# Kernel optimization log

Measured on AMD Instinct MI355X. Metric: run time of the kernel, lower is better.

The kernel has to match this reference:

```python
import jax, jax.numpy as jnp
import numpy as np


def setup_inputs() -> dict:
    key = jax.random.key(0)
    k1, k2 = jax.random.split(key)
    x = jax.random.normal(k1, (32, 64, 64, 64), dtype=jnp.float32)      # (B, D, H, W)
    weight = jax.random.uniform(k2, (64, 512), dtype=jnp.float32)       # (D, K), like torch.rand
    return {"x": x, "weight": weight}


def reference(x, weight):
    # Euclidean nearest-embedding (hyperbolic=False, bounded_measure=False).
    # argmin of ||x - e||_2 over codebook equals argmin of squared distance;
    # drop the ||x||^2 term (constant per location) for efficiency.
    # x: (B, D, H, W), weight: (D, K)
    scores = -2.0 * jnp.einsum('bdhw,dk->bhwk', x, weight) + jnp.sum(weight * weight, axis=0)  # (B,H,W,K)
    argmin = jnp.argmin(scores, axis=-1)                 # (B, H, W) int
    quantized = weight.T[argmin]                         # (B, H, W, D) codebook gather
    result = jnp.transpose(quantized, (0, 3, 1, 2))      # (B, D, H, W)
    return result, argmin
```

## Files before the change

kernel.cpp:

```cpp
#include <hip/hip_runtime.h>


typedef float  f32x4  __attribute__((ext_vector_type(4)));
typedef short  bf16x8 __attribute__((ext_vector_type(8)));

#define KK   512
#define DD   64
#define HWSZ 4096
#define NLOC (32*HWSZ)
#define LPB  512
#define TAU  1e-3f

static __device__ __forceinline__ short f2bf_rne(float f) {
    unsigned u = __float_as_uint(f);
    unsigned r = (u + 0x7FFFu + ((u >> 16) & 1u)) >> 16;
    return (short)r;
}

__global__ __launch_bounds__(1024, 4)
void ne_mfma(const float* __restrict__ x, const float* __restrict__ w,
             float* __restrict__ out_res, float* __restrict__ out_idx) {
    __shared__ __align__(16) short wt_hi[KK*DD];
    __shared__ __align__(16) short wt_lo[KK*DD];
    __shared__ __align__(16) float w2s[KK];
    __shared__ int k1s[LPB];

    const int tid  = threadIdx.x;
    const int lane = tid & 63;
    const int wv   = tid >> 6;
    const int col  = lane & 15;
    const int lgr  = lane >> 4;

    const int bloc0 = blockIdx.x * LPB;
    const int b     = bloc0 >> 12;
    const long xbase = (long)b * (DD*HWSZ);
    const int hw0   = bloc0 & 4095;

    char* wh_b = (char*)wt_hi;
    char* wl_b = (char*)wt_lo;

    {
        const int n = tid & 511;
        const int h = tid >> 9;
        #pragma unroll
        for (int gg = 0; gg < 4; ++gg) {
            const int g = h*4 + gg;
            bf16x8 hv, lv;
            #pragma unroll
            for (int j = 0; j < 8; ++j) {
                float v = w[(g*8 + j)*KK + n];
                unsigned bits = __float_as_uint(v);
                unsigned hb = bits & 0xFFFF0000u;
                hv[j] = (short)(hb >> 16);
                lv[j] = f2bf_rne(v - __uint_as_float(hb));
            }
            const int slot = g ^ (n & 7);
            *(bf16x8*)(wh_b + n*128 + slot*16) = hv;
            *(bf16x8*)(wl_b + n*128 + slot*16) = lv;
        }
        if (h == 0) {
            float w2 = 0.f;
            #pragma unroll
            for (int d = 0; d < DD; ++d) {
                float v = w[d*KK + n];
                w2 = fmaf(v, v, w2);
            }
            w2s[n] = w2;
        }
    }

    const int wloc0 = bloc0 + wv * 32;
    bf16x8 Xh0[2], Xl0[2], Xh1[2], Xl1[2];
    #pragma unroll
    for (int s = 0; s < 2; ++s) {
        const int hw = (wloc0 + s*16 + col) & 4095;
        #pragma unroll
        for (int c = 0; c < 2; ++c) {
            #pragma unroll
            for (int j = 0; j < 8; ++j) {
                const int d = c*32 + lgr*8 + j;
                float v = x[xbase + (long)d*HWSZ + hw];
                unsigned bits = __float_as_uint(v);
                unsigned hb = bits & 0xFFFF0000u;
                short hj = (short)(hb >> 16);
                short lj = f2bf_rne(v - __uint_as_float(hb));
                if (s == 0) { Xh0[c][j] = hj; Xl0[c][j] = lj; }
                else        { Xh1[c][j] = hj; Xl1[c][j] = lj; }
            }
        }
    }

    __syncthreads();

    float m1[2][4], m2[2][4]; int i1[2][4], i2[2][4];
    #pragma unroll
    for (int s = 0; s < 2; ++s)
        #pragma unroll
        for (int r = 0; r < 4; ++r) { m1[s][r] = 3.4e38f; m2[s][r] = 3.4e38f; i1[s][r] = 0; i2[s][r] = 0; }

    #pragma unroll 2
    for (int t = 0; t < 32; ++t) {
        const int n = t*16 + col;
        f32x4 acc0 = {0.f,0.f,0.f,0.f}, acc1 = {0.f,0.f,0.f,0.f};
        #pragma unroll
        for (int c = 0; c < 2; ++c) {
            const int off = (n*128 + (c*4 + lgr)*16) ^ ((n & 7) << 4);
            bf16x8 Wh = *(const bf16x8*)(wh_b + off);
            bf16x8 Wl = *(const bf16x8*)(wl_b + off);
            acc0 = __builtin_amdgcn_mfma_f32_16x16x32_bf16(Wl, Xh0[c], acc0, 0,0,0);
            acc0 = __builtin_amdgcn_mfma_f32_16x16x32_bf16(Wh, Xl0[c], acc0, 0,0,0);
            acc0 = __builtin_amdgcn_mfma_f32_16x16x32_bf16(Wh, Xh0[c], acc0, 0,0,0);
            acc1 = __builtin_amdgcn_mfma_f32_16x16x32_bf16(Wl, Xh1[c], acc1, 0,0,0);
            acc1 = __builtin_amdgcn_mfma_f32_16x16x32_bf16(Wh, Xl1[c], acc1, 0,0,0);
            acc1 = __builtin_amdgcn_mfma_f32_16x16x32_bf16(Wh, Xh1[c], acc1, 0,0,0);
        }
        const f32x4 w2v = *(const f32x4*)((const char*)w2s + t*64 + lgr*16);
        const int kb = t*16 + lgr*4;
        #pragma unroll
        for (int r = 0; r < 4; ++r) {
            {
                float sc = fmaf(-2.f, acc0[r], w2v[r]);
                bool c1 = sc < m1[0][r], c2 = sc < m2[0][r];
                m2[0][r] = c1 ? m1[0][r] : (c2 ? sc : m2[0][r]);
                i2[0][r] = c1 ? i1[0][r] : (c2 ? (kb+r) : i2[0][r]);
                m1[0][r] = c1 ? sc : m1[0][r];
                i1[0][r] = c1 ? (kb+r) : i1[0][r];
            }
            {
                float sc = fmaf(-2.f, acc1[r], w2v[r]);
                bool c1 = sc < m1[1][r], c2 = sc < m2[1][r];
                m2[1][r] = c1 ? m1[1][r] : (c2 ? sc : m2[1][r]);
                i2[1][r] = c1 ? i1[1][r] : (c2 ? (kb+r) : i2[1][r]);
                m1[1][r] = c1 ? sc : m1[1][r];
                i1[1][r] = c1 ? (kb+r) : i1[1][r];
            }
        }
    }

    #pragma unroll
    for (int s = 0; s < 2; ++s) {
        float a1 = m1[s][0], a2 = m2[s][0]; int j1 = i1[s][0], j2 = i2[s][0];
        #pragma unroll
        for (int r = 1; r < 4; ++r) {
            float b1v = m1[s][r], b2v = m2[s][r]; int jb1 = i1[s][r], jb2 = i2[s][r];
            bool bw = (b1v < a1) || (b1v == a1 && jb1 < j1);
            float w1 = bw ? b1v : a1;  int wj1 = bw ? jb1 : j1;
            float lo = bw ? a1  : b1v; int loj = bw ? j1  : jb1;
            float ws = bw ? b2v : a2;  int wsj = bw ? jb2 : j2;
            bool sw = (lo < ws) || (lo == ws && loj < wsj);
            a1 = w1; j1 = wj1;
            a2 = sw ? lo : ws; j2 = sw ? loj : wsj;
        }
        #pragma unroll
        for (int msk = 16; msk <= 32; msk <<= 1) {
            float b1v = __shfl_xor(a1, msk, 64);
            int   jb1 = __shfl_xor(j1, msk, 64);
            float b2v = __shfl_xor(a2, msk, 64);
            int   jb2 = __shfl_xor(j2, msk, 64);
            bool bw = (b1v < a1) || (b1v == a1 && jb1 < j1);
            float w1 = bw ? b1v : a1;  int wj1 = bw ? jb1 : j1;
            float lo = bw ? a1  : b1v; int loj = bw ? j1  : jb1;
            float ws = bw ? b2v : a2;  int wsj = bw ? jb2 : j2;
            bool sw = (lo < ws) || (lo == ws && loj < wsj);
            a1 = w1; j1 = wj1;
            a2 = sw ? lo : ws; j2 = sw ? loj : wsj;
        }
        if (lane < 16) {
            const int loc = wloc0 + s*16 + lane;
            int kf = j1;
            if (a2 - a1 < TAU) {
                const int hw = loc & 4095;
                double bd = 1e300; int bk = 1 << 30;
                for (int ci = 0; ci < 2; ++ci) {
                    int kk = ci ? j2 : j1;
                    double dot = 0.0, w2d = 0.0;
                    for (int d = 0; d < DD; ++d) {
                        double wvv = (double)w[(long)d*KK + kk];
                        dot = fma((double)x[xbase + (long)d*HWSZ + hw], wvv, dot);
                        w2d = fma(wvv, wvv, w2d);
                    }
                    double scd = fma(-2.0, dot, w2d);
                    if (scd < bd || (scd == bd && kk < bk)) { bd = scd; bk = kk; }
                }
                kf = bk;
            }
            k1s[loc - bloc0] = kf;
            out_idx[loc] = (float)kf;
        }
    }

    __syncthreads();

    {
        const int loc = tid & 511;
        const int dp  = tid >> 9;
        const int kf  = k1s[loc];
        const long ob = xbase + hw0 + loc;
        #pragma unroll
        for (int i = 0; i < 32; ++i) {
            const int d = i*2 + dp;
            out_res[ob + (long)d*HWSZ] = w[(long)d*KK + kf];
        }
    }
}

extern "C" void kernel_launch(void* const* d_in, const int* in_sizes, int n_in,
                              void* d_out, int out_size, void* d_ws, size_t ws_size,
                              hipStream_t stream) {
    const float* x = (const float*)d_in[0];
    const float* w = (const float*)d_in[1];
    float* out = (float*)d_out;
    float* out_res = out;
    float* out_idx = out + (NLOC * DD);
    ne_mfma<<<NLOC / LPB, 1024, 0, stream>>>(x, w, out_res, out_idx);
}
```

Before: 122.9 us.

## Pack score+index into sortable uint keys, fold w2 bias into MFMA accumulator

Scales the codebook by -2 and preloads the accumulator with ||w||^2+128, so scores are positive floats. Each score is then packed with its index into a single unsigned key, which makes top-3 tracking plain min/max operations. It also switches the hi/lo bf16 split to truncation, widens the tie tolerance, adds a third candidate to the fp64 refinement, and drops the shared-memory index buffer and block barrier by writing the gathered codebook vectors per wave. The masked key mantissa loses precision, which relies on the wider tau plus fp64 rechecks staying correct. A larger tau also sends more locations through the slow fp64 path.

```diff
diff --git a/kernel.cpp b/kernel.cpp
--- a/kernel.cpp
+++ b/kernel.cpp
@@ -9,13 +9,11 @@
 #define HWSZ 4096
 #define NLOC (32*HWSZ)
 #define LPB  512
-#define TAU  1e-3f
-
-static __device__ __forceinline__ short f2bf_rne(float f) {
-    unsigned u = __float_as_uint(f);
-    unsigned r = (u + 0x7FFFu + ((u >> 16) & 1u)) >> 16;
-    return (short)r;
-}
+#define TAU  4e-2f
+#define KEYMASK 0xFFFFFE00u
+
+static __device__ __forceinline__ unsigned umin(unsigned a, unsigned b) { return a < b ? a : b; }
+static __device__ __forceinline__ unsigned umax(unsigned a, unsigned b) { return a > b ? a : b; }
 
 __global__ __launch_bounds__(1024, 4)
 void ne_mfma(const float* __restrict__ x, const float* __restrict__ w,
@@ -23,7 +21,6 @@
     __shared__ __align__(16) short wt_hi[KK*DD];
     __shared__ __align__(16) short wt_lo[KK*DD];
     __shared__ __align__(16) float w2s[KK];
-    __shared__ int k1s[LPB];
 
     const int tid  = threadIdx.x;
     const int lane = tid & 63;
@@ -32,9 +29,8 @@
     const int lgr  = lane >> 4;
 
     const int bloc0 = blockIdx.x * LPB;
-    const int b     = bloc0 >> 12;
-    const long xbase = (long)b * (DD*HWSZ);
-    const int hw0   = bloc0 & 4095;
+    const int bidx  = bloc0 >> 12;
+    const long xbase = (long)bidx * (DD*HWSZ);
 
     char* wh_b = (char*)wt_hi;
     char* wl_b = (char*)wt_lo;
@@ -48,23 +44,20 @@
             bf16x8 hv, lv;
             #pragma unroll
             for (int j = 0; j < 8; ++j) {
-                float v = w[(g*8 + j)*KK + n];
+                float v = -2.0f * w[(g*8 + j)*KK + n];
                 unsigned bits = __float_as_uint(v);
-                unsigned hb = bits & 0xFFFF0000u;
-                hv[j] = (short)(hb >> 16);
-                lv[j] = f2bf_rne(v - __uint_as_float(hb));
+                hv[j] = (short)(bits >> 16);
+                float hi = __uint_as_float(bits & 0xFFFF0000u);
+                lv[j] = (short)(__float_as_uint(v - hi) >> 16);
             }
             const int slot = g ^ (n & 7);
             *(bf16x8*)(wh_b + n*128 + slot*16) = hv;
             *(bf16x8*)(wl_b + n*128 + slot*16) = lv;
         }
         if (h == 0) {
-            float w2 = 0.f;
+            float w2 = 128.0f;
             #pragma unroll
-            for (int d = 0; d < DD; ++d) {
-                float v = w[d*KK + n];
-                w2 = fmaf(v, v, w2);
-            }
+            for (int d = 0; d < DD; ++d) { float v = w[d*KK + n]; w2 = fmaf(v, v, w2); }
             w2s[n] = w2;
         }
     }
@@ -81,9 +74,9 @@
                 const int d = c*32 + lgr*8 + j;
                 float v = x[xbase + (long)d*HWSZ + hw];
                 unsigned bits = __float_as_uint(v);
-                unsigned hb = bits & 0xFFFF0000u;
-                short hj = (short)(hb >> 16);
-                short lj = f2bf_rne(v - __uint_as_float(hb));
+                short hj = (short)(bits >> 16);
+                float hi = __uint_as_float(bits & 0xFFFF0000u);
+                short lj = (short)(__float_as_uint(v - hi) >> 16);
                 if (s == 0) { Xh0[c][j] = hj; Xl0[c][j] = lj; }
                 else        { Xh1[c][j] = hj; Xl1[c][j] = lj; }
             }
@@ -92,114 +85,107 @@
 
     __syncthreads();
 
-    float m1[2][4], m2[2][4]; int i1[2][4], i2[2][4];
-    #pragma unroll
-    for (int s = 0; s < 2; ++s)
-        #pragma unroll
-        for (int r = 0; r < 4; ++r) { m1[s][r] = 3.4e38f; m2[s][r] = 3.4e38f; i1[s][r] = 0; i2[s][r] = 0; }
-
-    #pragma unroll 2
+    unsigned u1a = 0xFFFFFFFFu, u2a = 0xFFFFFFFFu, u3a = 0xFFFFFFFFu;
+    unsigned u1b = 0xFFFFFFFFu, u2b = 0xFFFFFFFFu, u3b = 0xFFFFFFFFu;
+
+    const int off0 = (col*128 + lgr*16)      ^ ((col & 7) << 4);
+    const int off1 = (col*128 + 64 + lgr*16) ^ ((col & 7) << 4);
+
+    #pragma unroll 4
     for (int t = 0; t < 32; ++t) {
-        const int n = t*16 + col;
-        f32x4 acc0 = {0.f,0.f,0.f,0.f}, acc1 = {0.f,0.f,0.f,0.f};
-        #pragma unroll
-        for (int c = 0; c < 2; ++c) {
-            const int off = (n*128 + (c*4 + lgr)*16) ^ ((n & 7) << 4);
-            bf16x8 Wh = *(const bf16x8*)(wh_b + off);
-            bf16x8 Wl = *(const bf16x8*)(wl_b + off);
-            acc0 = __builtin_amdgcn_mfma_f32_16x16x32_bf16(Wl, Xh0[c], acc0, 0,0,0);
-            acc0 = __builtin_amdgcn_mfma_f32_16x16x32_bf16(Wh, Xl0[c], acc0, 0,0,0);
-            acc0 = __builtin_amdgcn_mfma_f32_16x16x32_bf16(Wh, Xh0[c], acc0, 0,0,0);
-            acc1 = __builtin_amdgcn_mfma_f32_16x16x32_bf16(Wl, Xh1[c], acc1, 0,0,0);
-            acc1 = __builtin_amdgcn_mfma_f32_16x16x32_bf16(Wh, Xl1[c], acc1, 0,0,0);
-            acc1 = __builtin_amdgcn_mfma_f32_16x16x32_bf16(Wh, Xh1[c], acc1, 0,0,0);
-        }
         const f32x4 w2v = *(const f32x4*)((const char*)w2s + t*64 + lgr*16);
-        const int kb = t*16 + lgr*4;
+        f32x4 acc0 = w2v, acc1 = w2v;
+        {
+            bf16x8 Wh = *(const bf16x8*)(wh_b + t*2048 + off0);
+            bf16x8 Wl = *(const bf16x8*)(wl_b + t*2048 + off0);
+            acc0 = __builtin_amdgcn_mfma_f32_16x16x32_bf16(Wl, Xh0[0], acc0, 0,0,0);
+            acc0 = __builtin_amdgcn_mfma_f32_16x16x32_bf16(Wh, Xl0[0], acc0, 0,0,0);
+            acc0 = __builtin_amdgcn_mfma_f32_16x16x32_bf16(Wh, Xh0[0], acc0, 0,0,0);
+            acc1 = __builtin_amdgcn_mfma_f32_16x16x32_bf16(Wl, Xh1[0], acc1, 0,0,0);
+            acc1 = __builtin_amdgcn_mfma_f32_16x16x32_bf16(Wh, Xl1[0], acc1, 0,0,0);
+            acc1 = __builtin_amdgcn_mfma_f32_16x16x32_bf16(Wh, Xh1[0], acc1, 0,0,0);
+        }
+        {
+            bf16x8 Wh = *(const bf16x8*)(wh_b + t*2048 + off1);
+            bf16x8 Wl = *(const bf16x8*)(wl_b + t*2048 + off1);
+            acc0 = __builtin_amdgcn_mfma_f32_16x16x32_bf16(Wl, Xh0[1], acc0, 0,0,0);
+            acc0 = __builtin_amdgcn_mfma_f32_16x16x32_bf16(Wh, Xl0[1], acc0, 0,0,0);
+            acc0 = __builtin_amdgcn_mfma_f32_16x16x32_bf16(Wh, Xh0[1], acc0, 0,0,0);
+            acc1 = __builtin_amdgcn_mfma_f32_16x16x32_bf16(Wl, Xh1[1], acc1, 0,0,0);
+            acc1 = __builtin_amdgcn_mfma_f32_16x16x32_bf16(Wh, Xl1[1], acc1, 0,0,0);
+            acc1 = __builtin_amdgcn_mfma_f32_16x16x32_bf16(Wh, Xh1[1], acc1, 0,0,0);
+        }
+        const unsigned kb = (unsigned)(t*16 + lgr*4);
         #pragma unroll
         for (int r = 0; r < 4; ++r) {
             {
-                float sc = fmaf(-2.f, acc0[r], w2v[r]);
-                bool c1 = sc < m1[0][r], c2 = sc < m2[0][r];
-                m2[0][r] = c1 ? m1[0][r] : (c2 ? sc : m2[0][r]);
-                i2[0][r] = c1 ? i1[0][r] : (c2 ? (kb+r) : i2[0][r]);
-                m1[0][r] = c1 ? sc : m1[0][r];
-                i1[0][r] = c1 ? (kb+r) : i1[0][r];
+                unsigned key = (__float_as_uint(acc0[r]) & KEYMASK) | (kb + r);
+                unsigned m  = umax(u1a, key);  u1a = umin(u1a, key);
+                unsigned m2 = umax(u2a, m);    u2a = umin(u2a, m);
+                u3a = umin(u3a, m2);
             }
             {
-                float sc = fmaf(-2.f, acc1[r], w2v[r]);
-                bool c1 = sc < m1[1][r], c2 = sc < m2[1][r];
-                m2[1][r] = c1 ? m1[1][r] : (c2 ? sc : m2[1][r]);
-                i2[1][r] = c1 ? i1[1][r] : (c2 ? (kb+r) : i2[1][r]);
-                m1[1][r] = c1 ? sc : m1[1][r];
-                i1[1][r] = c1 ? (kb+r) : i1[1][r];
-            }
-        }
-    }
-
+                unsigned key = (__float_as_uint(acc1[r]) & KEYMASK) | (kb + r);
+                unsigned m  = umax(u1b, key);  u1b = umin(u1b, key);
+                unsigned m2 = umax(u2b, m);    u2b = umin(u2b, m);
+                u3b = umin(u3b, m2);
+            }
+        }
+    }
+
+    const unsigned U1[2] = {u1a, u1b}, U2[2] = {u2a, u2b}, U3[2] = {u3a, u3b};
     #pragma unroll
     for (int s = 0; s < 2; ++s) {
-        float a1 = m1[s][0], a2 = m2[s][0]; int j1 = i1[s][0], j2 = i2[s][0];
-        #pragma unroll
-        for (int r = 1; r < 4; ++r) {
-            float b1v = m1[s][r], b2v = m2[s][r]; int jb1 = i1[s][r], jb2 = i2[s][r];
-            bool bw = (b1v < a1) || (b1v == a1 && jb1 < j1);
-            float w1 = bw ? b1v : a1;  int wj1 = bw ? jb1 : j1;
-            float lo = bw ? a1  : b1v; int loj = bw ? j1  : jb1;
-            float ws = bw ? b2v : a2;  int wsj = bw ? jb2 : j2;
-            bool sw = (lo < ws) || (lo == ws && loj < wsj);
-            a1 = w1; j1 = wj1;
-            a2 = sw ? lo : ws; j2 = sw ? loj : wsj;
-        }
+        unsigned a1 = U1[s], a2 = U2[s], a3 = U3[s];
         #pragma unroll
         for (int msk = 16; msk <= 32; msk <<= 1) {
-            float b1v = __shfl_xor(a1, msk, 64);
-            int   jb1 = __shfl_xor(j1, msk, 64);
-            float b2v = __shfl_xor(a2, msk, 64);
-            int   jb2 = __shfl_xor(j2, msk, 64);
-            bool bw = (b1v < a1) || (b1v == a1 && jb1 < j1);
-            float w1 = bw ? b1v : a1;  int wj1 = bw ? jb1 : j1;
-            float lo = bw ? a1  : b1v; int loj = bw ? j1  : jb1;
-            float ws = bw ? b2v : a2;  int wsj = bw ? jb2 : j2;
-            bool sw = (lo < ws) || (lo == ws && loj < wsj);
-            a1 = w1; j1 = wj1;
-            a2 = sw ? lo : ws; j2 = sw ? loj : wsj;
-        }
+            unsigned b1 = (unsigned)__shfl_xor((int)a1, msk, 64);
+            unsigned b2 = (unsigned)__shfl_xor((int)a2, msk, 64);
+            unsigned b3 = (unsigned)__shfl_xor((int)a3, msk, 64);
+            unsigned c1 = umin(a1,b1), d1v = umax(a1,b1);
+            unsigned c2 = umin(a2,b2), d2v = umax(a2,b2);
+            unsigned n2 = umin(d1v, c2);
+            unsigned e  = umax(d1v, c2);
+            unsigned n3 = umin(umin(e, d2v), umin(a3, b3));
+            a1 = c1; a2 = n2; a3 = n3;
+        }
+        int kf = 0;
         if (lane < 16) {
-            const int loc = wloc0 + s*16 + lane;
-            int kf = j1;
-            if (a2 - a1 < TAU) {
-                const int hw = loc & 4095;
+            kf = (int)(a1 & 511u);
+            float f1 = __uint_as_float(a1 & KEYMASK);
+            float f2 = __uint_as_float(a2 & KEYMASK);
+            if (f2 - f1 < TAU) {
+                float f3 = __uint_as_float(a3 & KEYMASK);
+                int cands[3];
+                cands[0] = kf;
+                cands[1] = (int)(a2 & 511u);
+                cands[2] = (f3 - f1 < TAU) ? (int)(a3 & 511u) : -1;
+                const int hw = (wloc0 + s*16 + lane) & 4095;
                 double bd = 1e300; int bk = 1 << 30;
-                for (int ci = 0; ci < 2; ++ci) {
-                    int kk = ci ? j2 : j1;
-                    double dot = 0.0, w2d = 0.0;
-                    for (int d = 0; d < DD; ++d) {
-                        double wvv = (double)w[(long)d*KK + kk];
-                        dot = fma((double)x[xbase + (long)d*HWSZ + hw], wvv, dot);
-                        w2d = fma(wvv, wvv, w2d);
+                #pragma unroll
+                for (int ci = 0; ci < 3; ++ci) {
+                    int kk = cands[ci];
+                    if (kk >= 0) {
+                        double dot = 0.0, w2d = 0.0;
+                        for (int d = 0; d < DD; ++d) {
+                            double wvv = (double)w[(long)d*KK + kk];
+                            dot = fma((double)x[xbase + (long)d*HWSZ + hw], wvv, dot);
+                            w2d = fma(wvv, wvv, w2d);
+                        }
+                        double scd = fma(-2.0, dot, w2d);
+                        if (scd < bd || (scd == bd && kk < bk)) { bd = scd; bk = kk; }
                     }
-                    double scd = fma(-2.0, dot, w2d);
-                    if (scd < bd || (scd == bd && kk < bk)) { bd = scd; bk = kk; }
                 }
                 kf = bk;
             }
-            k1s[loc - bloc0] = kf;
-            out_idx[loc] = (float)kf;
-        }
-    }
-
-    __syncthreads();
-
-    {
-        const int loc = tid & 511;
-        const int dp  = tid >> 9;
-        const int kf  = k1s[loc];
-        const long ob = xbase + hw0 + loc;
-        #pragma unroll
-        for (int i = 0; i < 32; ++i) {
-            const int d = i*2 + dp;
-            out_res[ob + (long)d*HWSZ] = w[(long)d*KK + kf];
+            out_idx[wloc0 + s*16 + lane] = (float)kf;
+        }
+        const int kfb = __shfl(kf, col, 64);
+        const int hwb = (wloc0 + s*16) & 4095;
+        #pragma unroll
+        for (int i = 0; i < 16; ++i) {
+            const int d = lgr*16 + i;
+            out_res[xbase + (long)d*HWSZ + hwb + col] = w[d*KK + kfb];
         }
     }
 }
```

New measurement: 167.6 us. 1.36x slower.
